# Performance work log

Hardware: AMD Instinct MI355X
Metric: run time of the kernel (lower is better)

Reference implementation:

```python
import jax, jax.numpy as jnp
import numpy as np

H, DK = 4, 64
D = H * DK              # hidden_dim = 256
D_OUT = 64
L = 2
NT, ET = 2, 3
AUTHOR, PAPER = 0, 1                 # sorted ntypes: ['author','paper']
CITES, WRITES, WRITTEN_BY = 0, 1, 2  # sorted etypes: ['cites','writes','written-by']
NA, NPAPER = 20000, 40000
E_WB, E_W, E_C = 150000, 150000, 300000
SQRT_DK = float(np.sqrt(DK))
EPS = 1e-5


def setup_inputs() -> dict:
    key = jax.random.key(0)
    ks = jax.random.split(key, 24)
    s = 1.0 / np.sqrt(D)
    return {
        "x_author": jax.random.normal(ks[0], (NA, D), jnp.float32),
        "x_paper": jax.random.normal(ks[1], (NPAPER, D), jnp.float32),
        "ew_wb": jax.random.uniform(ks[2], (E_WB,), jnp.float32),
        "ew_w": jax.random.uniform(ks[3], (E_W,), jnp.float32),
        "ew_c": jax.random.uniform(ks[4], (E_C,), jnp.float32),
        "adapt_W": jax.random.normal(ks[5], (NT, D, D), jnp.float32) * s,
        "adapt_b": jnp.zeros((NT, D), jnp.float32),
        "kW": jax.random.normal(ks[6], (L, NT, D, D), jnp.float32) * s,
        "kb": jnp.zeros((L, NT, D), jnp.float32),
        "qW": jax.random.normal(ks[7], (L, NT, D, D), jnp.float32) * s,
        "qb": jnp.zeros((L, NT, D), jnp.float32),
        "mW": jax.random.normal(ks[8], (L, NT, D, D), jnp.float32) * s,
        "mb": jnp.zeros((L, NT, D), jnp.float32),
        "aW": jax.random.normal(ks[9], (L, NT, D, D), jnp.float32) * s,
        "ab": jnp.zeros((L, NT, D), jnp.float32),
        "w_pri": jnp.ones((L, ET, H), jnp.float32),
        "w_att": jax.random.normal(ks[10], (L, ET, H, DK, DK), jnp.float32) / np.sqrt(DK),
        "w_msg": jax.random.normal(ks[11], (L, ET, H, DK, DK), jnp.float32) / np.sqrt(DK),
        "skip": jnp.ones((L, ET), jnp.float32),
        "ln_g": jnp.ones((L, NT, D), jnp.float32),
        "ln_b": jnp.zeros((L, NT, D), jnp.float32),
        "out_W": jax.random.normal(ks[12], (D, D_OUT), jnp.float32) * s,
        "out_b": jnp.zeros((D_OUT,), jnp.float32),
        "src_wb": jax.random.randint(ks[13], (E_WB,), 0, NPAPER, jnp.int32),
        "dst_wb": jax.random.randint(ks[14], (E_WB,), 0, NA, jnp.int32),
        "src_w": jax.random.randint(ks[15], (E_W,), 0, NA, jnp.int32),
        "dst_w": jax.random.randint(ks[16], (E_W,), 0, NPAPER, jnp.int32),
        "src_c": jax.random.randint(ks[17], (E_C,), 0, NPAPER, jnp.int32),
        "dst_c": jax.random.randint(ks[18], (E_C,), 0, NPAPER, jnp.int32),
    }


def _ln(x, g, b):
    mu = x.mean(-1, keepdims=True)
    var = ((x - mu) ** 2).mean(-1, keepdims=True)
    return (x - mu) * jax.lax.rsqrt(var + EPS) * g + b


def _hgt_layer(feats, rels, kW, kb, qW, qb, mW, mb, aW, ab,
               w_pri, w_att, w_msg, skip, ln_g, ln_b):
    # feats: [x_author, x_paper]; per-ntype K/Q/M projections -> [N, H, DK]
    Ns = [f.shape[0] for f in feats]
    kbase = [(feats[t] @ kW[t] + kb[t]).reshape(-1, H, DK) for t in range(NT)]
    qbase = [(feats[t] @ qW[t] + qb[t]).reshape(-1, H, DK) for t in range(NT)]
    mbase = [(feats[t] @ mW[t] + mb[t]).reshape(-1, H, DK) for t in range(NT)]
    aggs = {}
    for (st, e, dt, src, dst, ew) in rels:
        k = jnp.einsum('nhd,hde->nhe', kbase[st], w_att[e])
        m = jnp.einsum('nhd,hde->nhe', mbase[st], w_msg[e])
        score = (qbase[dt][dst] * k[src]).sum(-1) * w_pri[e] / SQRT_DK  # [E, H]
        attn = jax.nn.sigmoid(score) * ew[:, None]
        msg = m[src] * attn[:, :, None]                                 # [E, H, DK]
        aggs[e] = jax.ops.segment_sum(msg, dst, num_segments=Ns[dt])
    # cross_reducer='mean': mean over relation aggregates per dst ntype
    t_author = aggs[WRITTEN_BY].reshape(Ns[AUTHOR], D)
    t_paper = ((aggs[WRITES] + aggs[CITES]) * 0.5).reshape(Ns[PAPER], D)
    new = []
    for nid, t in ((AUTHOR, t_author), (PAPER, t_paper)):
        alpha = jax.nn.sigmoid(skip[nid])  # skip indexed by n_id (as in source)
        tr = t @ aW[nid] + ab[nid]
        o = tr * alpha + feats[nid] * (1.0 - alpha)
        new.append(_ln(o, ln_g[nid], ln_b[nid]))
    return new


def _forward(x_author, x_paper, ew_wb, ew_w, ew_c,
             adapt_W, adapt_b, kW, kb, qW, qb, mW, mb, aW, ab,
             w_pri, w_att, w_msg, skip, ln_g, ln_b, out_W, out_b,
             src_wb, dst_wb, src_w, dst_w, src_c, dst_c):
    feats = [
        jax.nn.gelu(x_author @ adapt_W[AUTHOR] + adapt_b[AUTHOR], approximate=False),
        jax.nn.gelu(x_paper @ adapt_W[PAPER] + adapt_b[PAPER], approximate=False),
    ]
    rels = [
        (PAPER, WRITTEN_BY, AUTHOR, src_wb, dst_wb, ew_wb),
        (AUTHOR, WRITES, PAPER, src_w, dst_w, ew_w),
        (PAPER, CITES, PAPER, src_c, dst_c, ew_c),
    ]
    for l in range(L):
        feats = _hgt_layer(feats, rels, kW[l], kb[l], qW[l], qb[l], mW[l], mb[l],
                           aW[l], ab[l], w_pri[l], w_att[l], w_msg[l], skip[l],
                           ln_g[l], ln_b[l])
    return feats[PAPER] @ out_W + out_b  # out_key = 'paper'


def reference(x_author, x_paper, ew_wb, ew_w, ew_c,
              adapt_W, adapt_b, kW, kb, qW, qb, mW, mb, aW, ab,
              w_pri, w_att, w_msg, skip, ln_g, ln_b, out_W, out_b,
              src_wb, dst_wb, src_w, dst_w, src_c, dst_c):
    return _forward(x_author, x_paper, ew_wb, ew_w, ew_c,
                    adapt_W, adapt_b, kW, kb, qW, qb, mW, mb, aW, ab,
                    w_pri, w_att, w_msg, skip, ln_g, ln_b, out_W, out_b,
                    src_wb, dst_wb, src_w, dst_w, src_c, dst_c)
```

## Files before the change

### kernel.cpp

```cpp
#include <hip/hip_runtime.h>
#include <hip/hip_bf16.h>
#include <math.h>

using bf16 = __hip_bfloat16;

typedef __attribute__((ext_vector_type(8))) short short8;
typedef __attribute__((ext_vector_type(4))) float float4v;

static constexpr int kNA  = 20000;
static constexpr int kNP  = 40000;
static constexpr int kEWB = 150000;
static constexpr int kEW  = 150000;
static constexpr int kEC  = 300000;

static constexpr int kNSeg = 21;
static constexpr int kSegN[kNSeg] = {
  150000, 150000, 300000,
  131072, 512,
  262144, 1024,
  262144, 1024,
  262144, 1024,
  262144, 1024,
  24,
  98304, 98304,
  6, 1024, 1024,
  16384, 64
};
static constexpr size_t kOff(int s) {
  size_t o = 0;
  for (int i = 0; i < s; ++i) o += (size_t)kSegN[i];
  return o;
}
static constexpr size_t kCanonTotal = kOff(kNSeg);

struct CanonArgs {
  const void* src[kNSeg];
  int n[kNSeg];
  unsigned dstOff[kNSeg];
};
struct TransArgs {
  const bf16* src[10];
  bf16* dst[10];
};
struct GemmDesc {
  const short* wt;
  const bf16* bias;
  void* c;
  int ldc;
  int coff;
  int act;
  int otype;
  int pad;
};
struct MultiDesc { GemmDesc d[6]; };
struct ScanArgs {
  int* deg[3];
  int* offs[3];
  int* bsums;
  int N[3];
};

__device__ __forceinline__ float toF(float x) { return x; }
__device__ __forceinline__ float toF(bf16 x)  { return __bfloat162float(x); }
__device__ __forceinline__ float bits2f(unsigned short b) {
  unsigned int u = ((unsigned int)b) << 16;
  return __uint_as_float(u);
}
__device__ __forceinline__ float sigmoidf_(float x) { return 1.0f / (1.0f + expf(-x)); }
__device__ __forceinline__ float gelu_exact(float x) {
  return 0.5f * x * (1.0f + erff(x * 0.70710678118654752f));
}

__global__ __launch_bounds__(256) void detect_dtype(
    const unsigned* __restrict__ x, unsigned* __restrict__ flags)
{
  __shared__ int cnt;
  if (threadIdx.x == 0) cnt = 0;
  __syncthreads();
  unsigned w = x[threadIdx.x];
  unsigned e = (w >> 7) & 0xFFu;
  if (e >= 110u && e <= 140u) atomicAdd(&cnt, 1);
  __syncthreads();
  if (threadIdx.x == 0) {
    flags[0] = (cnt >= 128) ? 1u : 0u;
    flags[1] = 1u;
  }
}

__global__ __launch_bounds__(256) void canon_kernel(
    CanonArgs a, bf16* __restrict__ dst, const unsigned* __restrict__ flags)
{
  const int s = blockIdx.y;
  const int i = blockIdx.x * 256 + threadIdx.x;
  if (i >= a.n[s]) return;
  bf16 v;
  if (flags[0]) v = ((const bf16*)a.src[s])[i];
  else          v = __float2bfloat16(((const float*)a.src[s])[i]);
  dst[a.dstOff[s] + i] = v;
}

__global__ __launch_bounds__(256) void transpose_w(TransArgs ta)
{
  const int m = blockIdx.z;
  const short* src = (const short*)ta.src[m];
  short* dst = (short*)ta.dst[m];
  const int k0 = blockIdx.x * 64, n0 = blockIdx.y * 64;
  __shared__ short tile[64][65];
  const int tx = threadIdx.x & 63, ty = threadIdx.x >> 6;
  for (int i = ty; i < 64; i += 4)
    tile[i][tx] = src[(size_t)(k0 + i) * 256 + n0 + tx];
  __syncthreads();
  for (int i = ty; i < 64; i += 4)
    dst[(size_t)(n0 + i) * 256 + k0 + tx] = tile[tx][i];
}

__global__ __launch_bounds__(256) void csr_hist(
    const int* __restrict__ dst, int E, int* __restrict__ cnt)
{
  const int i = blockIdx.x * 256 + threadIdx.x;
  if (i < E) atomicAdd(&cnt[dst[i]], 1);
}

__global__ __launch_bounds__(256) void scan_l1(ScanArgs a)
{
  const int rel = blockIdx.y;
  const int N = a.N[rel];
  const int t = threadIdx.x;
  const int lane = t & 63;
  const int wid = t >> 6;
  const int i0 = blockIdx.x * 2048 + t * 8;
  const int* deg = a.deg[rel];
  int v[8];
  int T = 0;
  #pragma unroll
  for (int j = 0; j < 8; ++j) {
    v[j] = (i0 + j < N) ? deg[i0 + j] : 0;
    T += v[j];
  }
  int incl = T;
  #pragma unroll
  for (int off = 1; off < 64; off <<= 1) {
    const int u = __shfl_up(incl, off);
    if (lane >= off) incl += u;
  }
  __shared__ int wsum[4];
  if (lane == 63) wsum[wid] = incl;
  __syncthreads();
  int woff = 0;
  #pragma unroll
  for (int wp = 0; wp < 4; ++wp) if (wp < wid) woff += wsum[wp];
  int run = woff + incl - T;
  int* offs = a.offs[rel];
  #pragma unroll
  for (int j = 0; j < 8; ++j) {
    if (i0 + j < N) offs[i0 + j] = run;
    run += v[j];
  }
  if (t == 0)
    a.bsums[rel * 32 + blockIdx.x] = wsum[0] + wsum[1] + wsum[2] + wsum[3];
}

__global__ __launch_bounds__(64) void scan_l2(int* __restrict__ bsums,
                                              int* __restrict__ totals)
{
  const int rel = blockIdx.x;
  const int lane = threadIdx.x;
  const int v = (lane < 32) ? bsums[rel * 32 + lane] : 0;
  int incl = v;
  #pragma unroll
  for (int off = 1; off < 64; off <<= 1) {
    const int u = __shfl_up(incl, off);
    if (lane >= off) incl += u;
  }
  if (lane < 32) bsums[rel * 32 + lane] = incl - v;
  if (lane == 63) totals[rel] = incl;
}

__global__ __launch_bounds__(256) void scan_l3(ScanArgs a,
                                               const int* __restrict__ totals)
{
  const int rel = blockIdx.y;
  const int N = a.N[rel];
  const int i0 = blockIdx.x * 2048 + threadIdx.x * 8;
  const int boff = a.bsums[rel * 32 + blockIdx.x];
  int* offs = a.offs[rel];
  int* cur = a.deg[rel];
  #pragma unroll
  for (int j = 0; j < 8; ++j) {
    const int idx = i0 + j;
    if (idx < N) {
      const int o = offs[idx] + boff;
      offs[idx] = o;
      cur[idx] = o;
    }
  }
  if (blockIdx.x == 0 && threadIdx.x == 0) offs[N] = totals[rel];
}

__global__ __launch_bounds__(256) void csr_scatter(
    const int* __restrict__ dst, const int* __restrict__ src,
    const bf16* __restrict__ ew, int E, int* __restrict__ cur,
    int* __restrict__ srcs, bf16* __restrict__ ews)
{
  const int i = blockIdx.x * 256 + threadIdx.x;
  if (i >= E) return;
  const int p = atomicAdd(&cur[dst[i]], 1);
  srcs[p] = src[i];
  ews[p]  = ew[i];
}

__global__ __launch_bounds__(256) void combine_weights(
    const bf16* __restrict__ Wbig, const bf16* __restrict__ bbig,
    const bf16* __restrict__ wsm, bf16* __restrict__ KMT,
    bf16* __restrict__ kmb, int noff)
{
  const int blk = blockIdx.y;
  const int rc  = blockIdx.x;
  const int h = blk & 3;
  const int le = blk >> 2;
  const int e = le % 3;
  const int l = le / 3;
  const int st = (e == 1) ? 0 : 1;

  const short* Wsrc = (const short*)(Wbig + (size_t)(l * 2 + st) * 65536);
  const bf16*  bsrc = bbig + (size_t)(l * 2 + st) * 256;
  const short* wm   = (const short*)(wsm + ((size_t)(l * 3 + e) * 4 + h) * 4096);
  short* outT = (short*)(KMT + (size_t)(l * 3 + e) * 512 * 256);
  bf16* outb  = kmb + (size_t)(l * 3 + e) * 512;

  __shared__ short w[64][72];
  __shared__ short As[32][72];
  __shared__ short ot[64][40];

  const int t = threadIdx.x;
  {
    const int base = t * 16;
    const int r0 = base >> 6, c0 = base & 63;
    *(short8*)&w[r0][c0]     = *(const short8*)&wm[base];
    *(short8*)&w[r0][c0 + 8] = *(const short8*)&wm[base + 8];
  }
  {
    const int row = t >> 3;
    const int kc = (t & 7) * 8;
    *(short8*)&As[row][kc] =
        *(const short8*)&Wsrc[(size_t)(rc * 32 + row) * 256 + h * 64 + kc];
  }
  __syncthreads();

  const int j   = t & 63;
  const int sub = t >> 6;
  float accv[8] = {};
  #pragma unroll
  for (int d = 0; d < 64; ++d) {
    const float wd = bits2f((unsigned short)w[d][j]);
    #pragma unroll
    for (int r8 = 0; r8 < 8; ++r8)
      accv[r8] += bits2f((unsigned short)As[sub * 8 + r8][d]) * wd;
  }
  #pragma unroll
  for (int r8 = 0; r8 < 8; ++r8) {
    union { bf16 h; short s; } cv;
    cv.h = __float2bfloat16(accv[r8]);
    ot[j][sub * 8 + r8] = cv.s;
  }

  if (rc == 0 && t < 64) {
    float acc = 0.f;
    #pragma unroll
    for (int d = 0; d < 64; ++d)
      acc += toF(bsrc[h * 64 + d]) * bits2f((unsigned short)w[d][t]);
    outb[h * 64 + t + noff] = __float2bfloat16(acc);
  }
  __syncthreads();
  {
    const int nn = t >> 2;
    const int kx = (t & 3) * 8;
    short8 v;
    #pragma unroll
    for (int x = 0; x < 8; ++x) v[x] = ot[nn][kx + x];
    *(short8*)&outT[(size_t)(h * 64 + nn + noff) * 256 + rc * 32 + kx] = v;
  }
}

__global__ __launch_bounds__(256, 4) void mfma_gemm128(
    const void* __restrict__ A, const unsigned* __restrict__ aflag,
    MultiDesc md, int M, int ntiles, int nslab)
{
  __shared__ short As[128][72];
  __shared__ short Bs[128][72];
  const int lid = blockIdx.x;
  const int grp = lid / (8 * nslab);
  const int rem = lid - grp * 8 * nslab;
  const int slab = rem >> 3;
  const int tx = grp * 8 + (rem & 7);
  if (tx >= ntiles) return;
  const GemmDesc d = md.d[slab];
  const bool abf = (*aflag != 0u);
  const int t = threadIdx.x;
  const int bm = tx * 128;
  const int lane = t & 63;
  const int wid  = t >> 6;
  const int wm = (wid >> 1) * 64;
  const int wn = (wid & 1) * 64;
  const int col16 = lane & 15;
  const int quad  = lane >> 4;
  const int rr = t >> 3;
  const int kk = (t & 7) * 8;

  float4v acc[4][4];
  #pragma unroll
  for (int mi = 0; mi < 4; ++mi)
    #pragma unroll
    for (int ni = 0; ni < 4; ++ni) acc[mi][ni] = (float4v){0.f, 0.f, 0.f, 0.f};

  for (int k0 = 0; k0 < 256; k0 += 64) {
    #pragma unroll
    for (int it = 0; it < 4; ++it) {
      const int row = it * 32 + rr;
      const int grow = bm + row;
      short8 v = (short8){0, 0, 0, 0, 0, 0, 0, 0};
      if (grow < M) {
        if (abf) {
          v = *(const short8*)((const short*)A + (size_t)grow * 256 + k0 + kk);
        } else {
          const float* ap = (const float*)A + (size_t)grow * 256 + k0 + kk;
          #pragma unroll
          for (int j = 0; j < 8; ++j) {
            union { bf16 h; short s; } cv;
            cv.h = __float2bfloat16(ap[j]);
            v[j] = cv.s;
          }
        }
      }
      *(short8*)&As[row][kk] = v;
    }
    #pragma unroll
    for (int it = 0; it < 4; ++it) {
      const int n = it * 32 + rr;
      *(short8*)&Bs[n][kk] = *(const short8*)&d.wt[(size_t)n * 256 + k0 + kk];
    }
    __syncthreads();

    #pragma unroll
    for (int ks = 0; ks < 64; ks += 32) {
      short8 bfr[4];
      #pragma unroll
      for (int ni = 0; ni < 4; ++ni)
        bfr[ni] = *(const short8*)&Bs[wn + ni * 16 + col16][ks + quad * 8];
      #pragma unroll
      for (int mi = 0; mi < 4; ++mi) {
        const short8 afr = *(const short8*)&As[wm + mi * 16 + col16][ks + quad * 8];
        #pragma unroll
        for (int ni = 0; ni < 4; ++ni)
          acc[mi][ni] = __builtin_amdgcn_mfma_f32_16x16x32_bf16(afr, bfr[ni], acc[mi][ni], 0, 0, 0);
      }
    }
    __syncthreads();
  }

  #pragma unroll
  for (int ni = 0; ni < 4; ++ni) {
    const int col = wn + ni * 16 + col16;
    const float bc = toF(d.bias[col]);
    const int gcol = d.coff + col;
    #pragma unroll
    for (int mi = 0; mi < 4; ++mi) {
      #pragma unroll
      for (int r = 0; r < 4; ++r) {
        const int row = bm + wm + mi * 16 + quad * 4 + r;
        if (row < M) {
          float v = acc[mi][ni][r] + bc;
          if (d.act == 1) v = gelu_exact(v);
          const size_t idx = (size_t)row * d.ldc + gcol;
          if (d.otype == 0) ((bf16*)d.c)[idx] = __float2bfloat16(v);
          else              ((float*)d.c)[idx] = v;
        }
      }
    }
  }
}

__global__ __launch_bounds__(256) void gather_kernel(
    const bf16* __restrict__ q, const bf16* __restrict__ km,
    const int* __restrict__ srcs, const bf16* __restrict__ ews,
    const int* __restrict__ offs, const bf16* __restrict__ pri,
    bf16* __restrict__ agg, int Nd, int addPrev, float finalScale)
{
  const int lane = threadIdx.x & 63;
  const int wid  = threadIdx.x >> 6;
  const int node = blockIdx.x * 4 + wid;
  if (node >= Nd) return;
  const int h  = lane >> 5;
  const int sl = lane & 31;
  const float prih = toF(pri[sl >> 3]);

  union B8 { uint4 u; unsigned short s[8]; };
  B8 qv;
  qv.u = ((const uint4*)(q + (size_t)node * 256))[sl];
  float qf[8];
  #pragma unroll
  for (int j = 0; j < 8; ++j) qf[j] = bits2f(qv.s[j]);

  float acc[8] = {};
  const int beg = offs[node], end = offs[node + 1];
  for (int idx = beg + h; idx < end; idx += 2) {
    const int s = srcs[idx];
    const float w = toF(ews[idx]);
    B8 kb;
    kb.u = ((const uint4*)(km + (size_t)s * 512))[sl];
    float dot = 0.f;
    #pragma unroll
    for (int j = 0; j < 8; ++j) dot += qf[j] * bits2f(kb.s[j]);
    dot += __shfl_xor(dot, 1);
    dot += __shfl_xor(dot, 2);
    dot += __shfl_xor(dot, 4);
    const float a = w * sigmoidf_(dot * prih * 0.125f);
    B8 mb;
    mb.u = ((const uint4*)(km + (size_t)s * 512 + 256))[sl];
    #pragma unroll
    for (int j = 0; j < 8; ++j) acc[j] += bits2f(mb.s[j]) * a;
  }

  #pragma unroll
  for (int j = 0; j < 8; ++j) acc[j] += __shfl_xor(acc[j], 32);

  if (h == 0) {
    bf16* out = agg + (size_t)node * 256 + sl * 8;
    if (addPrev) {
      B8 pb;
      pb.u = *(const uint4*)out;
      #pragma unroll
      for (int j = 0; j < 8; ++j) acc[j] += bits2f(pb.s[j]);
    }
    B8 ov;
    #pragma unroll
    for (int j = 0; j < 8; ++j) {
      union { bf16 h; unsigned short u; } cv;
      cv.h = __float2bfloat16(acc[j] * finalScale);
      ov.s[j] = cv.u;
    }
    *(uint4*)out = ov.u;
  }
}

__global__ __launch_bounds__(256) void skip_ln(
    const float* __restrict__ tr, bf16* __restrict__ feat,
    const bf16* __restrict__ skipv, const bf16* __restrict__ g,
    const bf16* __restrict__ b, int N)
{
  const int lane = threadIdx.x & 63;
  const int wid  = threadIdx.x >> 6;
  const int node = blockIdx.x * 4 + wid;
  if (node >= N) return;
  const float alpha = sigmoidf_(toF(*skipv));
  const float4 t = ((const float4*)(tr + (size_t)node * 256))[lane];
  union B4 { uint2 u; unsigned short s[4]; };
  B4 fb;
  fb.u = ((const uint2*)(feat + (size_t)node * 256))[lane];
  float o[4];
  o[0] = t.x * alpha + bits2f(fb.s[0]) * (1.f - alpha);
  o[1] = t.y * alpha + bits2f(fb.s[1]) * (1.f - alpha);
  o[2] = t.z * alpha + bits2f(fb.s[2]) * (1.f - alpha);
  o[3] = t.w * alpha + bits2f(fb.s[3]) * (1.f - alpha);

  float sum = o[0] + o[1] + o[2] + o[3];
  #pragma unroll
  for (int off = 32; off; off >>= 1) sum += __shfl_xor(sum, off);
  const float mu = sum * (1.f / 256.f);

  float dd[4], sq = 0.f;
  #pragma unroll
  for (int j = 0; j < 4; ++j) { dd[j] = o[j] - mu; sq += dd[j] * dd[j]; }
  #pragma unroll
  for (int off = 32; off; off >>= 1) sq += __shfl_xor(sq, off);
  const float rs = rsqrtf(sq * (1.f / 256.f) + 1e-5f);

  bf16* fout = feat + (size_t)node * 256 + lane * 4;
  #pragma unroll
  for (int j = 0; j < 4; ++j) {
    float r = dd[j] * rs * toF(g[lane * 4 + j]) + toF(b[lane * 4 + j]);
    fout[j] = __float2bfloat16(r);
  }
}

__global__ __launch_bounds__(256) void out_gemm(
    const bf16* __restrict__ A, const bf16* __restrict__ W,
    const bf16* __restrict__ bias, void* __restrict__ out,
    const unsigned* __restrict__ flag, int M)
{
  __shared__ float Ws[64][64];
  const bool obf = (*flag != 0u);
  const int tid = threadIdx.x;
  const int row = blockIdx.x * 64 + (tid >> 2);
  const int c0 = (tid & 3) * 16;
  const int arow = (row < M) ? row : 0;
  const bf16* a = A + (size_t)arow * 256;
  float acc[16] = {};
  for (int k0 = 0; k0 < 256; k0 += 64) {
    for (int i = tid; i < 4096; i += 256)
      Ws[i >> 6][i & 63] = toF(W[(size_t)(k0 + (i >> 6)) * 64 + (i & 63)]);
    __syncthreads();
    for (int k = 0; k < 64; ++k) {
      const float av = toF(a[k0 + k]);
      #pragma unroll
      for (int j = 0; j < 16; ++j) acc[j] += av * Ws[k][c0 + j];
    }
    __syncthreads();
  }
  if (row < M) {
    #pragma unroll
    for (int j = 0; j < 16; ++j) {
      const float v = acc[j] + toF(bias[c0 + j]);
      const size_t idx = (size_t)row * 64 + c0 + j;
      if (obf) ((bf16*)out)[idx] = __float2bfloat16(v);
      else     ((float*)out)[idx] = v;
    }
  }
}

extern "C" void kernel_launch(void* const* d_in, const int* in_sizes, int n_in,
                              void* d_out, int out_size, void* d_ws, size_t ws_size,
                              hipStream_t stream) {
  const int* src_wb  = (const int*)d_in[23];
  const int* dst_wb  = (const int*)d_in[24];
  const int* src_w   = (const int*)d_in[25];
  const int* dst_w   = (const int*)d_in[26];
  const int* src_c   = (const int*)d_in[27];
  const int* dst_c   = (const int*)d_in[28];

  char* base = (char*)d_ws;
  unsigned* flags = (unsigned*)base;
  bf16* canon = (bf16*)(base + 256);
  char* p = base + 256 + (((size_t)kCanonTotal * 2 + 511) & ~(size_t)511);
  bf16* adWT = (bf16*)p;
  bf16* qWT  = adWT + (size_t)2 * 65536;
  bf16* aWT  = qWT  + (size_t)4 * 65536;
  bf16* KMeffT = aWT + (size_t)4 * 65536;
  bf16* kmbeT  = KMeffT + (size_t)6 * 512 * 256;
  char* pc = (char*)(((size_t)(kmbeT + 6 * 512) + 511) & ~(size_t)511);
  int* cur_wb  = (int*)pc;
  int* cur_w   = cur_wb + (kNA + 1);
  int* cur_c   = cur_w + (kNP + 1);
  int* offs_wb = cur_c + (kNP + 1);
  int* offs_w  = offs_wb + (kNA + 1);
  int* offs_c  = offs_w + (kNP + 1);
  int* srcs_wb = offs_c + (kNP + 1);
  int* srcs_w  = srcs_wb + kEWB;
  int* srcs_c  = srcs_w + kEW;
  bf16* ews_wb = (bf16*)(srcs_c + kEC);
  bf16* ews_w  = ews_wb + kEWB;
  bf16* ews_c  = ews_w + kEW;
  int* bsums   = (int*)(ews_c + kEC);
  int* totals  = bsums + 96;
  char* p2 = (char*)(((size_t)(totals + 3) + 511) & ~(size_t)511);
  bf16* fa  = (bf16*)p2;
  bf16* fp_ = fa + (size_t)kNA * 256;
  char* R   = (char*)(fp_ + (size_t)kNP * 256);
  bf16* qa   = (bf16*)R;
  bf16* qp   = qa + (size_t)kNA * 256;
  bf16* km_a = qp + (size_t)kNP * 256;
  bf16* km_p = km_a + (size_t)kNA * 512;
  float* tr_a = (float*)R;
  float* tr_p = tr_a + (size_t)kNA * 256;
  char* afterR = R + ((size_t)(kNA + kNP) * 256 + (size_t)(kNA + kNP) * 512) * sizeof(bf16);
  bf16* agg_a = (bf16*)afterR;
  bf16* agg_p = agg_a + (size_t)kNA * 256;

  const bf16* c_ew_wb = canon + kOff(0);
  const bf16* c_ew_w  = canon + kOff(1);
  const bf16* c_ew_c  = canon + kOff(2);
  const bf16* c_adW   = canon + kOff(3);
  const bf16* c_adb   = canon + kOff(4);
  const bf16* c_kW    = canon + kOff(5);
  const bf16* c_kb    = canon + kOff(6);
  const bf16* c_qW    = canon + kOff(7);
  const bf16* c_qb    = canon + kOff(8);
  const bf16* c_mW    = canon + kOff(9);
  const bf16* c_mb    = canon + kOff(10);
  const bf16* c_aW    = canon + kOff(11);
  const bf16* c_ab    = canon + kOff(12);
  const bf16* c_wpri  = canon + kOff(13);
  const bf16* c_watt  = canon + kOff(14);
  const bf16* c_wmsg  = canon + kOff(15);
  const bf16* c_skip  = canon + kOff(16);
  const bf16* c_lng   = canon + kOff(17);
  const bf16* c_lnb   = canon + kOff(18);
  const bf16* c_outW  = canon + kOff(19);
  const bf16* c_outb  = canon + kOff(20);

  const unsigned* fIn = flags + 0;
  const unsigned* f1  = flags + 1;

  detect_dtype<<<1, 256, 0, stream>>>((const unsigned*)d_in[0], flags);

  CanonArgs ca;
  for (int s = 0; s < kNSeg; ++s) { ca.n[s] = kSegN[s]; ca.dstOff[s] = (unsigned)kOff(s); }
  const int srcIdx[kNSeg] = {2,3,4, 5,6, 7,8, 9,10, 11,12, 13,14, 15, 16,17, 18,19,20, 21,22};
  for (int s = 0; s < kNSeg; ++s) ca.src[s] = d_in[srcIdx[s]];
  canon_kernel<<<dim3(1172, kNSeg), 256, 0, stream>>>(ca, canon, flags);

  TransArgs ta;
  ta.src[0] = c_adW;              ta.dst[0] = adWT;
  ta.src[1] = c_adW + 65536;      ta.dst[1] = adWT + 65536;
  for (int m = 0; m < 4; ++m) { ta.src[2 + m] = c_qW + (size_t)m * 65536; ta.dst[2 + m] = qWT + (size_t)m * 65536; }
  for (int m = 0; m < 4; ++m) { ta.src[6 + m] = c_aW + (size_t)m * 65536; ta.dst[6 + m] = aWT + (size_t)m * 65536; }
  transpose_w<<<dim3(4, 4, 10), 256, 0, stream>>>(ta);

  hipMemsetAsync(cur_wb, 0, (size_t)((kNA + 1) + 2 * (kNP + 1)) * 4, stream);
  csr_hist<<<(kEWB + 255) / 256, 256, 0, stream>>>(dst_wb, kEWB, cur_wb);
  csr_hist<<<(kEW  + 255) / 256, 256, 0, stream>>>(dst_w,  kEW,  cur_w);
  csr_hist<<<(kEC  + 255) / 256, 256, 0, stream>>>(dst_c,  kEC,  cur_c);
  ScanArgs sa;
  sa.deg[0] = cur_wb;  sa.offs[0] = offs_wb; sa.N[0] = kNA;
  sa.deg[1] = cur_w;   sa.offs[1] = offs_w;  sa.N[1] = kNP;
  sa.deg[2] = cur_c;   sa.offs[2] = offs_c;  sa.N[2] = kNP;
  sa.bsums = bsums;
  scan_l1<<<dim3(32, 3), 256, 0, stream>>>(sa);
  scan_l2<<<3, 64, 0, stream>>>(bsums, totals);
  scan_l3<<<dim3(20, 3), 256, 0, stream>>>(sa, totals);
  csr_scatter<<<(kEWB + 255) / 256, 256, 0, stream>>>(dst_wb, src_wb, c_ew_wb, kEWB, cur_wb, srcs_wb, ews_wb);
  csr_scatter<<<(kEW  + 255) / 256, 256, 0, stream>>>(dst_w,  src_w,  c_ew_w,  kEW,  cur_w,  srcs_w,  ews_w);
  csr_scatter<<<(kEC  + 255) / 256, 256, 0, stream>>>(dst_c,  src_c,  c_ew_c,  kEC,  cur_c,  srcs_c,  ews_c);

  combine_weights<<<dim3(8, 24), 256, 0, stream>>>(c_kW, c_kb, c_watt, KMeffT, kmbeT, 0);
  combine_weights<<<dim3(8, 24), 256, 0, stream>>>(c_mW, c_mb, c_wmsg, KMeffT, kmbeT, 256);

  auto sgrid = [](int m, int nslab) {
    const int nt = (m + 127) / 128;
    return dim3((unsigned)(((nt + 7) / 8) * 8 * nslab));
  };
  auto ntl = [](int m) { return (m + 127) / 128; };
  auto mkd = [](const bf16* wt, const bf16* bias, void* c, int ldc, int coff,
                int act, int otype) {
    GemmDesc g;
    g.wt = (const short*)wt; g.bias = bias; g.c = c; g.ldc = ldc;
    g.coff = coff; g.act = act; g.otype = otype; g.pad = 0;
    return g;
  };

  {
    MultiDesc md{};
    md.d[0] = mkd(adWT,                c_adb,        fa, 256, 0,   1, 0);
    md.d[1] = mkd(adWT + 128 * 256,    c_adb + 128,  fa, 256, 128, 1, 0);
    mfma_gemm128<<<sgrid(kNA, 2), 256, 0, stream>>>(d_in[0], fIn, md, kNA, ntl(kNA), 2);
    md.d[0] = mkd(adWT + 65536,        c_adb + 256,  fp_, 256, 0,   1, 0);
    md.d[1] = mkd(adWT + 65536 + 128 * 256, c_adb + 384, fp_, 256, 128, 1, 0);
    mfma_gemm128<<<sgrid(kNP, 2), 256, 0, stream>>>(d_in[1], fIn, md, kNP, ntl(kNP), 2);
  }

  for (int l = 0; l < 2; ++l) {
    const bf16* qW_a = qWT + (size_t)(l * 2 + 0) * 65536;
    const bf16* qW_p = qWT + (size_t)(l * 2 + 1) * 65536;
    const bf16* qb_a = c_qb + (l * 2 + 0) * 256;
    const bf16* qb_p = c_qb + (l * 2 + 1) * 256;
    const bf16* KM_c  = KMeffT + (size_t)(l * 3 + 0) * 512 * 256;
    const bf16* KM_w  = KMeffT + (size_t)(l * 3 + 1) * 512 * 256;
    const bf16* KM_wb = KMeffT + (size_t)(l * 3 + 2) * 512 * 256;
    const bf16* kb_c  = kmbeT + (l * 3 + 0) * 512;
    const bf16* kb_w  = kmbeT + (l * 3 + 1) * 512;
    const bf16* kb_wb = kmbeT + (l * 3 + 2) * 512;

    {
      MultiDesc md{};
      md.d[0] = mkd(qW_a,             qb_a,        qa,   256, 0,   0, 0);
      md.d[1] = mkd(qW_a + 128 * 256, qb_a + 128,  qa,   256, 128, 0, 0);
      for (int s = 0; s < 4; ++s)
        md.d[2 + s] = mkd(KM_w + (size_t)s * 128 * 256, kb_w + s * 128, km_a, 512, s * 128, 0, 0);
      mfma_gemm128<<<sgrid(kNA, 6), 256, 0, stream>>>(fa, f1, md, kNA, ntl(kNA), 6);
    }
    {
      MultiDesc md{};
      md.d[0] = mkd(qW_p,             qb_p,        qp,   256, 0,   0, 0);
      md.d[1] = mkd(qW_p + 128 * 256, qb_p + 128,  qp,   256, 128, 0, 0);
      for (int s = 0; s < 4; ++s)
        md.d[2 + s] = mkd(KM_wb + (size_t)s * 128 * 256, kb_wb + s * 128, km_p, 512, s * 128, 0, 0);
      mfma_gemm128<<<sgrid(kNP, 6), 256, 0, stream>>>(fp_, f1, md, kNP, ntl(kNP), 6);
    }

    gather_kernel<<<(kNA + 3) / 4, 256, 0, stream>>>(
        qa, km_p, srcs_wb, ews_wb, offs_wb, c_wpri + (l * 3 + 2) * 4,
        agg_a, kNA, 0, 1.f);
    gather_kernel<<<(kNP + 3) / 4, 256, 0, stream>>>(
        qp, km_a, srcs_w, ews_w, offs_w, c_wpri + (l * 3 + 1) * 4,
        agg_p, kNP, 0, 1.f);

    {
      MultiDesc md{};
      for (int s = 0; s < 4; ++s)
        md.d[s] = mkd(KM_c + (size_t)s * 128 * 256, kb_c + s * 128, km_p, 512, s * 128, 0, 0);
      mfma_gemm128<<<sgrid(kNP, 4), 256, 0, stream>>>(fp_, f1, md, kNP, ntl(kNP), 4);
    }
    gather_kernel<<<(kNP + 3) / 4, 256, 0, stream>>>(
        qp, km_p, srcs_c, ews_c, offs_c, c_wpri + (l * 3 + 0) * 4,
        agg_p, kNP, 1, 0.5f);

    {
      const bf16* aW_a = aWT + (size_t)(l * 2 + 0) * 65536;
      const bf16* aW_p = aWT + (size_t)(l * 2 + 1) * 65536;
      MultiDesc md{};
      md.d[0] = mkd(aW_a,             c_ab + (l * 2 + 0) * 256,       tr_a, 256, 0,   0, 1);
      md.d[1] = mkd(aW_a + 128 * 256, c_ab + (l * 2 + 0) * 256 + 128, tr_a, 256, 128, 0, 1);
      mfma_gemm128<<<sgrid(kNA, 2), 256, 0, stream>>>(agg_a, f1, md, kNA, ntl(kNA), 2);
      md.d[0] = mkd(aW_p,             c_ab + (l * 2 + 1) * 256,       tr_p, 256, 0,   0, 1);
      md.d[1] = mkd(aW_p + 128 * 256, c_ab + (l * 2 + 1) * 256 + 128, tr_p, 256, 128, 0, 1);
      mfma_gemm128<<<sgrid(kNP, 2), 256, 0, stream>>>(agg_p, f1, md, kNP, ntl(kNP), 2);
    }

    skip_ln<<<kNA / 4, 256, 0, stream>>>(
        tr_a, fa,  c_skip + l * 3 + 0, c_lng + (l * 2 + 0) * 256, c_lnb + (l * 2 + 0) * 256, kNA);
    skip_ln<<<kNP / 4, 256, 0, stream>>>(
        tr_p, fp_, c_skip + l * 3 + 1, c_lng + (l * 2 + 1) * 256, c_lnb + (l * 2 + 1) * 256, kNP);
  }

  out_gemm<<<kNP / 64, 256, 0, stream>>>(fp_, c_outW, c_outb, d_out, fIn, kNP);
}
```

Before: 904.8 us.

## Batch per-relation kernels into grouped launches and reorder gather stages

```diff
diff --git a/kernel.cpp b/kernel.cpp
--- a/kernel.cpp
+++ b/kernel.cpp
@@ -45,19 +45,47 @@
 struct GemmDesc {
   const short* wt;
   const bf16* bias;
+  const void* A;
   void* c;
   int ldc;
   int coff;
   int act;
   int otype;
-  int pad;
+  int M;
+  int ntiles;
 };
-struct MultiDesc { GemmDesc d[6]; };
+struct MultiDesc { GemmDesc d[10]; };
 struct ScanArgs {
   int* deg[3];
   int* offs[3];
   int* bsums;
   int N[3];
+};
+struct HistArgs {
+  const int* dst[3];
+  int* cnt[3];
+  int E[3];
+};
+struct ScatArgs {
+  const int* dst[3];
+  const int* src[3];
+  const bf16* ew[3];
+  int* cur[3];
+  int* srcs[3];
+  bf16* ews[3];
+  int E[3];
+};
+struct GatherDesc {
+  const bf16* q;
+  const bf16* km;
+  const int* srcs;
+  const bf16* ews;
+  const int* offs;
+  const bf16* pri;
+  bf16* agg;
+  int Nd;
+  int addPrev;
+  float scale;
 };
 
 __device__ __forceinline__ float toF(float x) { return x; }
@@ -114,11 +142,11 @@
     dst[(size_t)(n0 + i) * 256 + k0 + tx] = tile[tx][i];
 }
 
-__global__ __launch_bounds__(256) void csr_hist(
-    const int* __restrict__ dst, int E, int* __restrict__ cnt)
-{
+__global__ __launch_bounds__(256) void csr_hist(HistArgs h)
+{
+  const int rel = blockIdx.y;
   const int i = blockIdx.x * 256 + threadIdx.x;
-  if (i < E) atomicAdd(&cnt[dst[i]], 1);
+  if (i < h.E[rel]) atomicAdd(&h.cnt[rel][h.dst[rel][i]], 1);
 }
 
 __global__ __launch_bounds__(256) void scan_l1(ScanArgs a)
@@ -197,16 +225,14 @@
   if (blockIdx.x == 0 && threadIdx.x == 0) offs[N] = totals[rel];
 }
 
-__global__ __launch_bounds__(256) void csr_scatter(
-    const int* __restrict__ dst, const int* __restrict__ src,
-    const bf16* __restrict__ ew, int E, int* __restrict__ cur,
-    int* __restrict__ srcs, bf16* __restrict__ ews)
-{
+__global__ __launch_bounds__(256) void csr_scatter(ScatArgs s)
+{
+  const int rel = blockIdx.y;
   const int i = blockIdx.x * 256 + threadIdx.x;
-  if (i >= E) return;
-  const int p = atomicAdd(&cur[dst[i]], 1);
-  srcs[p] = src[i];
-  ews[p]  = ew[i];
+  if (i >= s.E[rel]) return;
+  const int p = atomicAdd(&s.cur[rel][s.dst[rel][i]], 1);
+  s.srcs[rel][p] = s.src[rel][i];
+  s.ews[rel][p]  = s.ew[rel][i];
 }
 
 __global__ __launch_bounds__(256) void combine_weights(
@@ -283,8 +309,7 @@
 }
 
 __global__ __launch_bounds__(256, 4) void mfma_gemm128(
-    const void* __restrict__ A, const unsigned* __restrict__ aflag,
-    MultiDesc md, int M, int ntiles, int nslab)
+    const unsigned* __restrict__ aflag, MultiDesc md, int nslab)
 {
   __shared__ short As[128][72];
   __shared__ short Bs[128][72];
@@ -293,9 +318,10 @@
   const int rem = lid - grp * 8 * nslab;
   const int slab = rem >> 3;
   const int tx = grp * 8 + (rem & 7);
-  if (tx >= ntiles) return;
   const GemmDesc d = md.d[slab];
+  if (tx >= d.ntiles) return;
   const bool abf = (*aflag != 0u);
+  const int M = d.M;
   const int t = threadIdx.x;
   const int bm = tx * 128;
   const int lane = t & 63;
@@ -321,9 +347,9 @@
       short8 v = (short8){0, 0, 0, 0, 0, 0, 0, 0};
       if (grow < M) {
         if (abf) {
-          v = *(const short8*)((const short*)A + (size_t)grow * 256 + k0 + kk);
+          v = *(const short8*)((const short*)d.A + (size_t)grow * 256 + k0 + kk);
         } else {
-          const float* ap = (const float*)A + (size_t)grow * 256 + k0 + kk;
+          const float* ap = (const float*)d.A + (size_t)grow * 256 + k0 + kk;
           #pragma unroll
           for (int j = 0; j < 8; ++j) {
             union { bf16 h; short s; } cv;
@@ -380,34 +406,34 @@
   }
 }
 
-__global__ __launch_bounds__(256) void gather_kernel(
-    const bf16* __restrict__ q, const bf16* __restrict__ km,
-    const int* __restrict__ srcs, const bf16* __restrict__ ews,
-    const int* __restrict__ offs, const bf16* __restrict__ pri,
-    bf16* __restrict__ agg, int Nd, int addPrev, float finalScale)
-{
+__global__ __launch_bounds__(256) void gather_fused(
+    GatherDesc da, GatherDesc db, int blocksA)
+{
+  const GatherDesc d = (blockIdx.x < (unsigned)blocksA) ? da : db;
+  const int bidx = (blockIdx.x < (unsigned)blocksA) ? blockIdx.x
+                                                    : blockIdx.x - blocksA;
   const int lane = threadIdx.x & 63;
   const int wid  = threadIdx.x >> 6;
-  const int node = blockIdx.x * 4 + wid;
-  if (node >= Nd) return;
+  const int node = bidx * 4 + wid;
+  if (node >= d.Nd) return;
   const int h  = lane >> 5;
   const int sl = lane & 31;
-  const float prih = toF(pri[sl >> 3]);
+  const float prih = toF(d.pri[sl >> 3]);
 
   union B8 { uint4 u; unsigned short s[8]; };
   B8 qv;
-  qv.u = ((const uint4*)(q + (size_t)node * 256))[sl];
+  qv.u = ((const uint4*)(d.q + (size_t)node * 256))[sl];
   float qf[8];
   #pragma unroll
   for (int j = 0; j < 8; ++j) qf[j] = bits2f(qv.s[j]);
 
   float acc[8] = {};
-  const int beg = offs[node], end = offs[node + 1];
+  const int beg = d.offs[node], end = d.offs[node + 1];
   for (int idx = beg + h; idx < end; idx += 2) {
-    const int s = srcs[idx];
-    const float w = toF(ews[idx]);
+    const int s = d.srcs[idx];
+    const float w = toF(d.ews[idx]);
     B8 kb;
-    kb.u = ((const uint4*)(km + (size_t)s * 512))[sl];
+    kb.u = ((const uint4*)(d.km + (size_t)s * 512))[sl];
     float dot = 0.f;
     #pragma unroll
     for (int j = 0; j < 8; ++j) dot += qf[j] * bits2f(kb.s[j]);
@@ -416,7 +442,7 @@
     dot += __shfl_xor(dot, 4);
     const float a = w * sigmoidf_(dot * prih * 0.125f);
     B8 mb;
-    mb.u = ((const uint4*)(km + (size_t)s * 512 + 256))[sl];
+    mb.u = ((const uint4*)(d.km + (size_t)s * 512 + 256))[sl];
     #pragma unroll
     for (int j = 0; j < 8; ++j) acc[j] += bits2f(mb.s[j]) * a;
   }
@@ -425,8 +451,10 @@
   for (int j = 0; j < 8; ++j) acc[j] += __shfl_xor(acc[j], 32);
 
   if (h == 0) {
-    bf16* out = agg + (size_t)node * 256 + sl * 8;
-    if (addPrev) {
+    bf16* out = d.agg + (size_t)node * 256 + sl * 8;
+    #pragma unroll
+    for (int j = 0; j < 8; ++j) acc[j] *= d.scale;
+    if (d.addPrev) {
       B8 pb;
       pb.u = *(const uint4*)out;
       #pragma unroll
@@ -436,23 +464,29 @@
     #pragma unroll
     for (int j = 0; j < 8; ++j) {
       union { bf16 h; unsigned short u; } cv;
-      cv.h = __float2bfloat16(acc[j] * finalScale);
+      cv.h = __float2bfloat16(acc[j]);
       ov.s[j] = cv.u;
     }
     *(uint4*)out = ov.u;
   }
 }
 
-__global__ __launch_bounds__(256) void skip_ln(
-    const float* __restrict__ tr, bf16* __restrict__ feat,
-    const bf16* __restrict__ skipv, const bf16* __restrict__ g,
-    const bf16* __restrict__ b, int N)
+__global__ __launch_bounds__(256) void skip_ln2(
+    const float* __restrict__ trA, bf16* __restrict__ featA,
+    const bf16* __restrict__ skA, const bf16* __restrict__ gA_, const bf16* __restrict__ bA,
+    const float* __restrict__ trP, bf16* __restrict__ featP,
+    const bf16* __restrict__ skP, const bf16* __restrict__ gP, const bf16* __restrict__ bP,
+    int NA, int Ntot)
 {
   const int lane = threadIdx.x & 63;
   const int wid  = threadIdx.x >> 6;
-  const int node = blockIdx.x * 4 + wid;
-  if (node >= N) return;
-  const float alpha = sigmoidf_(toF(*skipv));
+  int node = blockIdx.x * 4 + wid;
+  if (node >= Ntot) return;
+  const float* tr; bf16* feat; const bf16 *sk, *g, *b;
+  if (node < NA) { tr = trA; feat = featA; sk = skA; g = gA_; b = bA; }
+  else { node -= NA; tr = trP; feat = featP; sk = skP; g = gP; b = bP; }
+
+  const float alpha = sigmoidf_(toF(*sk));
   const float4 t = ((const float4*)(tr + (size_t)node * 256))[lane];
   union B4 { uint2 u; unsigned short s[4]; };
   B4 fb;
@@ -607,9 +641,11 @@
   transpose_w<<<dim3(4, 4, 10), 256, 0, stream>>>(ta);
 
   hipMemsetAsync(cur_wb, 0, (size_t)((kNA + 1) + 2 * (kNP + 1)) * 4, stream);
-  csr_hist<<<(kEWB + 255) / 256, 256, 0, stream>>>(dst_wb, kEWB, cur_wb);
-  csr_hist<<<(kEW  + 255) / 256, 256, 0, stream>>>(dst_w,  kEW,  cur_w);
-  csr_hist<<<(kEC  + 255) / 256, 256, 0, stream>>>(dst_c,  kEC,  cur_c);
+  HistArgs ha;
+  ha.dst[0] = dst_wb; ha.cnt[0] = cur_wb; ha.E[0] = kEWB;
+  ha.dst[1] = dst_w;  ha.cnt[1] = cur_w;  ha.E[1] = kEW;
+  ha.dst[2] = dst_c;  ha.cnt[2] = cur_c;  ha.E[2] = kEC;
+  csr_hist<<<dim3((kEC + 255) / 256, 3), 256, 0, stream>>>(ha);
   ScanArgs sa;
   sa.deg[0] = cur_wb;  sa.offs[0] = offs_wb; sa.N[0] = kNA;
   sa.deg[1] = cur_w;   sa.offs[1] = offs_w;  sa.N[1] = kNP;
@@ -618,34 +654,38 @@
   scan_l1<<<dim3(32, 3), 256, 0, stream>>>(sa);
   scan_l2<<<3, 64, 0, stream>>>(bsums, totals);
   scan_l3<<<dim3(20, 3), 256, 0, stream>>>(sa, totals);
-  csr_scatter<<<(kEWB + 255) / 256, 256, 0, stream>>>(dst_wb, src_wb, c_ew_wb, kEWB, cur_wb, srcs_wb, ews_wb);
-  csr_scatter<<<(kEW  + 255) / 256, 256, 0, stream>>>(dst_w,  src_w,  c_ew_w,  kEW,  cur_w,  srcs_w,  ews_w);
-  csr_scatter<<<(kEC  + 255) / 256, 256, 0, stream>>>(dst_c,  src_c,  c_ew_c,  kEC,  cur_c,  srcs_c,  ews_c);
+  ScatArgs sc;
+  sc.dst[0] = dst_wb; sc.src[0] = src_wb; sc.ew[0] = c_ew_wb; sc.cur[0] = cur_wb;
+  sc.srcs[0] = srcs_wb; sc.ews[0] = ews_wb; sc.E[0] = kEWB;
+  sc.dst[1] = dst_w;  sc.src[1] = src_w;  sc.ew[1] = c_ew_w;  sc.cur[1] = cur_w;
+  sc.srcs[1] = srcs_w;  sc.ews[1] = ews_w;  sc.E[1] = kEW;
+  sc.dst[2] = dst_c;  sc.src[2] = src_c;  sc.ew[2] = c_ew_c;  sc.cur[2] = cur_c;
+  sc.srcs[2] = srcs_c;  sc.ews[2] = ews_c;  sc.E[2] = kEC;
+  csr_scatter<<<dim3((kEC + 255) / 256, 3), 256, 0, stream>>>(sc);
 
   combine_weights<<<dim3(8, 24), 256, 0, stream>>>(c_kW, c_kb, c_watt, KMeffT, kmbeT, 0);
   combine_weights<<<dim3(8, 24), 256, 0, stream>>>(c_mW, c_mb, c_wmsg, KMeffT, kmbeT, 256);
 
-  auto sgrid = [](int m, int nslab) {
-    const int nt = (m + 127) / 128;
-    return dim3((unsigned)(((nt + 7) / 8) * 8 * nslab));
+  const int ntA = (kNA + 127) / 128;
+  const int ntP = (kNP + 127) / 128;
+  auto sgrid = [](int maxnt, int nslab) {
+    return dim3((unsigned)(((maxnt + 7) / 8) * 8 * nslab));
   };
-  auto ntl = [](int m) { return (m + 127) / 128; };
-  auto mkd = [](const bf16* wt, const bf16* bias, void* c, int ldc, int coff,
-                int act, int otype) {
+  auto mkd = [](const bf16* wt, const bf16* bias, const void* A, void* c,
+                int ldc, int coff, int act, int otype, int M, int ntiles) {
     GemmDesc g;
-    g.wt = (const short*)wt; g.bias = bias; g.c = c; g.ldc = ldc;
-    g.coff = coff; g.act = act; g.otype = otype; g.pad = 0;
+    g.wt = (const short*)wt; g.bias = bias; g.A = A; g.c = c; g.ldc = ldc;
+    g.coff = coff; g.act = act; g.otype = otype; g.M = M; g.ntiles = ntiles;
     return g;
   };
 
   {
     MultiDesc md{};
-    md.d[0] = mkd(adWT,                c_adb,        fa, 256, 0,   1, 0);
-    md.d[1] = mkd(adWT + 128 * 256,    c_adb + 128,  fa, 256, 128, 1, 0);
-    mfma_gemm128<<<sgrid(kNA, 2), 256, 0, stream>>>(d_in[0], fIn, md, kNA, ntl(kNA), 2);
-    md.d[0] = mkd(adWT + 65536,        c_adb + 256,  fp_, 256, 0,   1, 0);
-    md.d[1] = mkd(adWT + 65536 + 128 * 256, c_adb + 384, fp_, 256, 128, 1, 0);
-    mfma_gemm128<<<sgrid(kNP, 2), 256, 0, stream>>>(d_in[1], fIn, md, kNP, ntl(kNP), 2);
+    md.d[0] = mkd(adWT,                 c_adb,       d_in[0], fa,  256, 0,   1, 0, kNA, ntA);
+    md.d[1] = mkd(adWT + 128 * 256,     c_adb + 128, d_in[0], fa,  256, 128, 1, 0, kNA, ntA);
+    md.d[2] = mkd(adWT + 65536,         c_adb + 256, d_in[1], fp_, 256, 0,   1, 0, kNP, ntP);
+    md.d[3] = mkd(adWT + 65536 + 128 * 256, c_adb + 384, d_in[1], fp_, 256, 128, 1, 0, kNP, ntP);
+    mfma_gemm128<<<sgrid(ntP, 4), 256, 0, stream>>>(fIn, md, 4);
   }
 
   for (int l = 0; l < 2; ++l) {
@@ -662,54 +702,50 @@
 
     {
       MultiDesc md{};
-      md.d[0] = mkd(qW_a,             qb_a,        qa,   256, 0,   0, 0);
-      md.d[1] = mkd(qW_a + 128 * 256, qb_a + 128,  qa,   256, 128, 0, 0);
+      md.d[0] = mkd(qW_p,             qb_p,       fp_, qp,   256, 0,   0, 0, kNP, ntP);
+      md.d[1] = mkd(qW_p + 128 * 256, qb_p + 128, fp_, qp,   256, 128, 0, 0, kNP, ntP);
       for (int s = 0; s < 4; ++s)
-        md.d[2 + s] = mkd(KM_w + (size_t)s * 128 * 256, kb_w + s * 128, km_a, 512, s * 128, 0, 0);
-      mfma_gemm128<<<sgrid(kNA, 6), 256, 0, stream>>>(fa, f1, md, kNA, ntl(kNA), 6);
+        md.d[2 + s] = mkd(KM_c + (size_t)s * 128 * 256, kb_c + s * 128, fp_, km_p, 512, s * 128, 0, 0, kNP, ntP);
+      mfma_gemm128<<<sgrid(ntP, 6), 256, 0, stream>>>(f1, md, 6);
+    }
+    {
+      GatherDesc dc{qp, km_p, srcs_c, ews_c, offs_c, c_wpri + (l * 3 + 0) * 4,
+                    agg_p, kNP, 0, 0.5f};
+      GatherDesc dz{}; dz.Nd = 0;
+      gather_fused<<<(kNP + 3) / 4, 256, 0, stream>>>(dc, dz, (kNP + 3) / 4);
     }
     {
       MultiDesc md{};
-      md.d[0] = mkd(qW_p,             qb_p,        qp,   256, 0,   0, 0);
-      md.d[1] = mkd(qW_p + 128 * 256, qb_p + 128,  qp,   256, 128, 0, 0);
+      md.d[0] = mkd(qW_a,             qb_a,       fa, qa,   256, 0,   0, 0, kNA, ntA);
+      md.d[1] = mkd(qW_a + 128 * 256, qb_a + 128, fa, qa,   256, 128, 0, 0, kNA, ntA);
       for (int s = 0; s < 4; ++s)
-        md.d[2 + s] = mkd(KM_wb + (size_t)s * 128 * 256, kb_wb + s * 128, km_p, 512, s * 128, 0, 0);
-      mfma_gemm128<<<sgrid(kNP, 6), 256, 0, stream>>>(fp_, f1, md, kNP, ntl(kNP), 6);
-    }
-
-    gather_kernel<<<(kNA + 3) / 4, 256, 0, stream>>>(
-        qa, km_p, srcs_wb, ews_wb, offs_wb, c_wpri + (l * 3 + 2) * 4,
-        agg_a, kNA, 0, 1.f);
-    gather_kernel<<<(kNP + 3) / 4, 256, 0, stream>>>(
-        qp, km_a, srcs_w, ews_w, offs_w, c_wpri + (l * 3 + 1) * 4,
-        agg_p, kNP, 0, 1.f);
-
+        md.d[2 + s] = mkd(KM_w + (size_t)s * 128 * 256, kb_w + s * 128, fa, km_a, 512, s * 128, 0, 0, kNA, ntA);
+      for (int s = 0; s < 4; ++s)
+        md.d[6 + s] = mkd(KM_wb + (size_t)s * 128 * 256, kb_wb + s * 128, fp_, km_p, 512, s * 128, 0, 0, kNP, ntP);
+      mfma_gemm128<<<sgrid(ntP, 10), 256, 0, stream>>>(f1, md, 10);
+    }
     {
-      MultiDesc md{};
-      for (int s = 0; s < 4; ++s)
-        md.d[s] = mkd(KM_c + (size_t)s * 128 * 256, kb_c + s * 128, km_p, 512, s * 128, 0, 0);
-      mfma_gemm128<<<sgrid(kNP, 4), 256, 0, stream>>>(fp_, f1, md, kNP, ntl(kNP), 4);
-    }
-    gather_kernel<<<(kNP + 3) / 4, 256, 0, stream>>>(
-        qp, km_p, srcs_c, ews_c, offs_c, c_wpri + (l * 3 + 0) * 4,
-        agg_p, kNP, 1, 0.5f);
-
+      GatherDesc dwb{qa, km_p, srcs_wb, ews_wb, offs_wb, c_wpri + (l * 3 + 2) * 4,
+                     agg_a, kNA, 0, 1.f};
+      GatherDesc dw{qp, km_a, srcs_w, ews_w, offs_w, c_wpri + (l * 3 + 1) * 4,
+                    agg_p, kNP, 1, 0.5f};
+      const int bA = (kNA + 3) / 4;
+      gather_fused<<<bA + (kNP + 3) / 4, 256, 0, stream>>>(dwb, dw, bA);
+    }
     {
       const bf16* aW_a = aWT + (size_t)(l * 2 + 0) * 65536;
       const bf16* aW_p = aWT + (size_t)(l * 2 + 1) * 65536;
       MultiDesc md{};
-      md.d[0] = mkd(aW_a,             c_ab + (l * 2 + 0) * 256,       tr_a, 256, 0,   0, 1);
-      md.d[1] = mkd(aW_a + 128 * 256, c_ab + (l * 2 + 0) * 256 + 128, tr_a, 256, 128, 0, 1);
-      mfma_gemm128<<<sgrid(kNA, 2), 256, 0, stream>>>(agg_a, f1, md, kNA, ntl(kNA), 2);
-      md.d[0] = mkd(aW_p,             c_ab + (l * 2 + 1) * 256,       tr_p, 256, 0,   0, 1);
-      md.d[1] = mkd(aW_p + 128 * 256, c_ab + (l * 2 + 1) * 256 + 128, tr_p, 256, 128, 0, 1);
-      mfma_gemm128<<<sgrid(kNP, 2), 256, 0, stream>>>(agg_p, f1, md, kNP, ntl(kNP), 2);
-    }
-
-    skip_ln<<<kNA / 4, 256, 0, stream>>>(
-        tr_a, fa,  c_skip + l * 3 + 0, c_lng + (l * 2 + 0) * 256, c_lnb + (l * 2 + 0) * 256, kNA);
-    skip_ln<<<kNP / 4, 256, 0, stream>>>(
-        tr_p, fp_, c_skip + l * 3 + 1, c_lng + (l * 2 + 1) * 256, c_lnb + (l * 2 + 1) * 256, kNP);
+      md.d[0] = mkd(aW_a,             c_ab + (l * 2 + 0) * 256,       agg_a, tr_a, 256, 0,   0, 1, kNA, ntA);
+      md.d[1] = mkd(aW_a + 128 * 256, c_ab + (l * 2 + 0) * 256 + 128, agg_a, tr_a, 256, 128, 0, 1, kNA, ntA);
+      md.d[2] = mkd(aW_p,             c_ab + (l * 2 + 1) * 256,       agg_p, tr_p, 256, 0,   0, 1, kNP, ntP);
+      md.d[3] = mkd(aW_p + 128 * 256, c_ab + (l * 2 + 1) * 256 + 128, agg_p, tr_p, 256, 128, 0, 1, kNP, ntP);
+      mfma_gemm128<<<sgrid(ntP, 4), 256, 0, stream>>>(f1, md, 4);
+    }
+    skip_ln2<<<(kNA + kNP) / 4, 256, 0, stream>>>(
+        tr_a, fa,  c_skip + l * 3 + 0, c_lng + (l * 2 + 0) * 256, c_lnb + (l * 2 + 0) * 256,
+        tr_p, fp_, c_skip + l * 3 + 1, c_lng + (l * 2 + 1) * 256, c_lnb + (l * 2 + 1) * 256,
+        kNA, kNA + kNP);
   }
 
   out_gemm<<<kNP / 64, 256, 0, stream>>>(fp_, c_outW, c_outb, d_out, fIn, kNP);
```

New measurement: 853.9 us. -5.6%, faster.
